# Kernel optimization log

Measured on AMD Instinct MI355X. Metric: run time of the kernel, lower is better.

## Reference

```python
import jax, jax.numpy as jnp
import numpy as np

B, S, D, H, L, V = 4, 1024, 1024, 16, 4, 32000
DH = D // H
DFF = 4 * D
PAD = 0
EPS = 1e-5


def setup_inputs() -> dict:
    key = jax.random.key(0)
    ks = jax.random.split(key, 10)
    std = 0.02
    inp = {
        'token_batch': jax.random.randint(ks[0], (B, S), 0, V),
        'E': jax.random.normal(ks[1], (V, D), jnp.float32) * std,
        'P': jax.random.normal(ks[2], (S, D), jnp.float32) * std,
        'Wq': jax.random.normal(ks[3], (L, H, D, DH), jnp.float32) * std,
        'bq': jnp.zeros((L, H, DH), jnp.float32),
        'Wk': jax.random.normal(ks[4], (L, H, D, DH), jnp.float32) * std,
        'bk': jnp.zeros((L, H, DH), jnp.float32),
        'Wv': jax.random.normal(ks[5], (L, H, D, DH), jnp.float32) * std,
        'bv': jnp.zeros((L, H, DH), jnp.float32),
        'W0': jax.random.normal(ks[6], (L, D, D), jnp.float32) * std,
        'b0': jnp.zeros((L, D), jnp.float32),
        'ln1_g': jnp.ones((L, D), jnp.float32),
        'ln1_b': jnp.zeros((L, D), jnp.float32),
        'ln2_g': jnp.ones((L, D), jnp.float32),
        'ln2_b': jnp.zeros((L, D), jnp.float32),
        'W1': jax.random.normal(ks[7], (L, D, DFF), jnp.float32) * std,
        'b1': jnp.zeros((L, DFF), jnp.float32),
        'W2': jax.random.normal(ks[8], (L, DFF, D), jnp.float32) * std,
        'b2': jnp.zeros((L, D), jnp.float32),
    }
    return inp


def _layernorm(x, g, b):
    m = jnp.mean(x, axis=-1, keepdims=True)
    v = jnp.mean(jnp.square(x - m), axis=-1, keepdims=True)
    return (x - m) * jax.lax.rsqrt(v + EPS) * g + b


def reference(token_batch, E, P, Wq, bq, Wk, bk, Wv, bv, W0, b0,
              ln1_g, ln1_b, ln2_g, ln2_b, W1, b1, W2, b2):
    scale = 1.0 / np.sqrt(DH)
    pad_mask = token_batch != PAD                         # [B,S]
    causal = jnp.tril(jnp.ones((S, S), bool))
    # combined causal + query-pad + key-pad mask, [B,S,S]
    mask = causal[None] & pad_mask[:, :, None] & pad_mask[:, None, :]

    X = E[token_batch] + P[None, :S]                      # [B,S,D] (dropout is eval no-op)

    def block(X, p):
        wq, bq_, wk, bk_, wv, bv_, w0, b0_, g1, be1, g2, be2, w1, bb1, w2, bb2 = p
        h = _layernorm(X, g1, be1)
        Q = jnp.einsum('bsd,hde->bhse', h, wq) + bq_[None, :, None, :]
        K = jnp.einsum('bsd,hde->bhse', h, wk) + bk_[None, :, None, :]
        Vv = jnp.einsum('bsd,hde->bhse', h, wv) + bv_[None, :, None, :]
        scores = jnp.einsum('bhse,bhte->bhst', Q, K) * scale
        scores = jnp.where(mask[:, None], scores, -1e9)
        w = jax.nn.softmax(scores, axis=-1)
        attn = jnp.einsum('bhst,bhte->bhse', w, Vv)       # [B,H,S,DH]
        attn = attn.transpose(0, 2, 1, 3).reshape(B, S, D)
        X = attn @ w0 + b0_ + X
        h = _layernorm(X, g2, be2)
        X = jax.nn.relu(h @ w1 + bb1) @ w2 + bb2 + X
        return X, None

    X, _ = jax.lax.scan(block, X, (Wq, bq, Wk, bk, Wv, bv, W0, b0,
                                   ln1_g, ln1_b, ln2_g, ln2_b, W1, b1, W2, b2))
    logits = X @ E.T                                      # tied-weight output head
    return logits
```

## Files before the change

### kernel.cpp

```cpp
#include <hip/hip_runtime.h>
#include <hip/hip_bf16.h>
#include <stdint.h>

#define BB   4
#define SS   1024
#define DD   1024
#define HH   16
#define LL   4
#define VV   32000
#define DHH  64
#define DFFN 4096
#define BSZ  4096

typedef __hip_bfloat16 bf16_t;
typedef _Float16 f16_t;
typedef __attribute__((ext_vector_type(8))) _Float16 f16x8;
typedef __attribute__((ext_vector_type(4))) float    f4v;

typedef __attribute__((address_space(1))) const void gvoid_t;
typedef __attribute__((address_space(3))) void       svoid_t;

static_assert(sizeof(f16_t) == 2, "f16 size");

__device__ __forceinline__ void gl2lds16(const f16_t* g, f16_t* l) {
  __builtin_amdgcn_global_load_lds(
      reinterpret_cast<gvoid_t*>(reinterpret_cast<uintptr_t>(g)),
      reinterpret_cast<svoid_t*>(static_cast<uint32_t>(reinterpret_cast<uintptr_t>(l))),
      16, 0, 0);
}

__device__ __forceinline__ float readf(const void* src, long i, int m) {
  if (m == 1) return __bfloat162float(((const bf16_t*)src)[i]);
  if (m == 2) return (float)((const f16_t*)src)[i];
  return ((const float*)src)[i];
}

__global__ void detect_k(const unsigned int* __restrict__ src, int* __restrict__ flag) {
  __shared__ int cnt;
  int tid = threadIdx.x;
  if (tid == 0) cnt = 0;
  __syncthreads();
  int c = 0;
  for (int i = tid; i < 1024; i += 256) {
    unsigned int w = src[i] & 0xffffu;
    unsigned int e = (w >> 7) & 0xffu;
    c += (e >= 96 && e <= 150) ? 1 : 0;
  }
  atomicAdd(&cnt, c);
  __syncthreads();
  if (tid == 0) *flag = (cnt >= 512) ? 1 : 0;
}

__global__ __launch_bounds__(256) void conv_f16_k(const void* __restrict__ src, f16_t* __restrict__ dst,
                                                  long n, const int* __restrict__ flag, int mode) {
  int m = (mode < 0) ? *flag : mode;
  long i = (long)blockIdx.x * blockDim.x + threadIdx.x;
  long stride = (long)gridDim.x * blockDim.x;
  for (; i < n; i += stride) dst[i] = (f16_t)readf(src, i, m);
}

__global__ __launch_bounds__(256) void conv_f32_k(const void* __restrict__ src, float* __restrict__ dst,
                                                  long n, const int* __restrict__ flag) {
  int m = *flag;
  long i = (long)blockIdx.x * blockDim.x + threadIdx.x;
  long stride = (long)gridDim.x * blockDim.x;
  for (; i < n; i += stride) dst[i] = readf(src, i, m);
}

__global__ __launch_bounds__(256) void transpose_k(const void* __restrict__ src, f16_t* __restrict__ dst,
                                                   int R, int C, const int* __restrict__ flag, int mode,
                                                   long dstL, int zper, long dstH) {
  int m = (mode < 0) ? *flag : mode;
  __shared__ float t[32][33];
  int tx = threadIdx.x, ty = threadIdx.y;
  long sbase = (long)blockIdx.z * R * C;
  long dbase = (long)(blockIdx.z / zper) * dstL + (long)(blockIdx.z % zper) * dstH;
  int c = blockIdx.x * 32 + tx;
#pragma unroll
  for (int i = 0; i < 4; ++i) {
    int r = blockIdx.y * 32 + ty + i * 8;
    t[ty + i * 8][tx] = (r < R && c < C) ? readf(src, sbase + (long)r * C + c, m) : 0.f;
  }
  __syncthreads();
#pragma unroll
  for (int i = 0; i < 4; ++i) {
    int oc = blockIdx.x * 32 + ty + i * 8;
    int orw = blockIdx.y * 32 + tx;
    if (oc < C && orw < R) dst[dbase + (long)oc * R + orw] = (f16_t)t[tx][ty + i * 8];
  }
}

__global__ __launch_bounds__(256) void embed_k(const int* __restrict__ tok, const f16_t* __restrict__ E,
                                               const f16_t* __restrict__ P, float* __restrict__ X) {
  int mrow = blockIdx.x;
  int s = mrow & (SS - 1);
  long eb = (long)tok[mrow] * DD;
  long pb = (long)s * DD;
  int d = threadIdx.x * 4;
  float4 o;
  o.x = (float)E[eb + d + 0] + (float)P[pb + d + 0];
  o.y = (float)E[eb + d + 1] + (float)P[pb + d + 1];
  o.z = (float)E[eb + d + 2] + (float)P[pb + d + 2];
  o.w = (float)E[eb + d + 3] + (float)P[pb + d + 3];
  ((float4*)(X + (long)mrow * DD))[threadIdx.x] = o;
}

__global__ __launch_bounds__(256) void ln_k(const float* __restrict__ X, const float* __restrict__ g,
                                            const float* __restrict__ be, f16_t* __restrict__ out) {
  __shared__ float red1[4], red2[4];
  int row = blockIdx.x, tid = threadIdx.x;
  float4 x = ((const float4*)(X + (long)row * DD))[tid];
  float s = x.x + x.y + x.z + x.w;
#pragma unroll
  for (int o = 32; o; o >>= 1) s += __shfl_down(s, o);
  if ((tid & 63) == 0) red1[tid >> 6] = s;
  __syncthreads();
  float mean = (red1[0] + red1[1] + red1[2] + red1[3]) * (1.f / DD);
  float d0 = x.x - mean, d1 = x.y - mean, d2 = x.z - mean, d3 = x.w - mean;
  float v = d0 * d0 + d1 * d1 + d2 * d2 + d3 * d3;
#pragma unroll
  for (int o = 32; o; o >>= 1) v += __shfl_down(v, o);
  if ((tid & 63) == 0) red2[tid >> 6] = v;
  __syncthreads();
  float rs = rsqrtf((red2[0] + red2[1] + red2[2] + red2[3]) * (1.f / DD) + 1e-5f);
  int d = tid * 4;
  union { ushort4 u4; f16_t h[4]; } o;
  o.h[0] = (f16_t)(d0 * rs * g[d + 0] + be[d + 0]);
  o.h[1] = (f16_t)(d1 * rs * g[d + 1] + be[d + 1]);
  o.h[2] = (f16_t)(d2 * rs * g[d + 2] + be[d + 2]);
  o.h[3] = (f16_t)(d3 * rs * g[d + 3] + be[d + 3]);
  ((ushort4*)(out + (long)row * DD))[tid] = o.u4;
}

__global__ __launch_bounds__(256) void softmax_k(const f16_t* __restrict__ sc, f16_t* __restrict__ pr,
                                                 const int* __restrict__ tok, int z0) {
  __shared__ float red1[4], red2[4];
  int s = blockIdx.x, zl = blockIdx.y, tid = threadIdx.x;
  int z = z0 + zl;
  int b = z & (BB - 1);
  const f16_t* srow = sc + ((long)zl * SS + s) * SS;
  f16_t* prow = pr + ((long)zl * SS + s) * SS;
  const int* tb = tok + b * SS;
  if (tb[s] == 0) {
    for (int k = tid; k < SS; k += 256) prow[k] = (f16_t)(1.0f / SS);
    return;
  }
  float val[4]; bool vld[4];
  float mx = -3e38f;
#pragma unroll
  for (int i = 0; i < 4; ++i) {
    int k = tid + i * 256;
    bool valid = (k <= s) && (tb[k] != 0);
    float v = valid ? (float)srow[k] * 0.125f : -3e38f;
    val[i] = v; vld[i] = valid;
    mx = fmaxf(mx, v);
  }
#pragma unroll
  for (int o = 32; o; o >>= 1) mx = fmaxf(mx, __shfl_down(mx, o));
  if ((tid & 63) == 0) red1[tid >> 6] = mx;
  __syncthreads();
  mx = fmaxf(fmaxf(red1[0], red1[1]), fmaxf(red1[2], red1[3]));
  float e[4]; float sum = 0.f;
#pragma unroll
  for (int i = 0; i < 4; ++i) { e[i] = vld[i] ? __expf(val[i] - mx) : 0.f; sum += e[i]; }
#pragma unroll
  for (int o = 32; o; o >>= 1) sum += __shfl_down(sum, o);
  if ((tid & 63) == 0) red2[tid >> 6] = sum;
  __syncthreads();
  float inv = 1.0f / (red2[0] + red2[1] + red2[2] + red2[3]);
#pragma unroll
  for (int i = 0; i < 4; ++i) prow[tid + i * 256] = (f16_t)(e[i] * inv);
}

struct GemmP {
  const f16_t* A; const f16_t* B; void* C;
  int M, N, K, lda, ldb, ldc;
  long sAz, sBz;
  int z0, zdiv, czmode;
  long sCz1, sCz2;
  const float* bias;
  long bstr;
  const float* resid;
  const int* flag;
};

template <int EPI, bool SKIPU, int BN>
__global__ __launch_bounds__(256) void gemm_bt(GemmP p) {
  int bx = blockIdx.x, by = blockIdx.y, bz = blockIdx.z;
  if (SKIPU && bx > by) return;
  constexpr int NJ = BN / 32;
  __shared__ __align__(16) f16_t la[128 * 32];
  __shared__ __align__(16) f16_t lb[BN * 32];
  int tid = threadIdx.x;
  const f16_t* Ab = p.A + (long)bz * p.sAz;
  const f16_t* Bb = p.B + (long)bz * p.sBz;

  int r0 = tid >> 2;
  int c8 = (tid & 3) << 3;
  long ar0 = (long)by * 128 + r0;
  long ar1 = ar0 + 64;
  int brow0 = bx * BN + r0;      if (brow0 > p.N - 1) brow0 = p.N - 1;
  const f16_t* ag0 = Ab + ar0 * p.lda + c8;
  const f16_t* ag1 = Ab + ar1 * p.lda + c8;
  const f16_t* bg0 = Bb + (long)brow0 * p.ldb + c8;
  const f16_t* bg1 = nullptr;
  if constexpr (BN == 128) {
    int brow1 = bx * BN + 64 + r0; if (brow1 > p.N - 1) brow1 = p.N - 1;
    bg1 = Bb + (long)brow1 * p.ldb + c8;
  }
  f16_t* la0 = la + tid * 8; f16_t* la1 = la + 2048 + tid * 8;
  f16_t* lb0 = lb + tid * 8; f16_t* lb1 = lb + 2048 + tid * 8;

  int w = tid >> 6, l = tid & 63;
  int wm = (w >> 1) << 6, wn = (w & 1) * (BN / 2);
  int lr = l & 15, q = l >> 4;

  f4v acc[4][NJ];
  f4v zero = {0.f, 0.f, 0.f, 0.f};
#pragma unroll
  for (int i = 0; i < 4; ++i)
#pragma unroll
    for (int j = 0; j < NJ; ++j) acc[i][j] = zero;

  int nk = p.K >> 5;
  for (int kt = 0; kt < nk; ++kt) {
    __syncthreads();
    long ko = (long)kt << 5;
    gl2lds16(ag0 + ko, la0);
    gl2lds16(ag1 + ko, la1);
    gl2lds16(bg0 + ko, lb0);
    if constexpr (BN == 128) gl2lds16(bg1 + ko, lb1);
    __syncthreads();
    f16x8 af[4], bfr[NJ];
#pragma unroll
    for (int i = 0; i < 4; ++i) af[i] = *(const f16x8*)(la + (wm + i * 16 + lr) * 32 + q * 8);
#pragma unroll
    for (int j = 0; j < NJ; ++j) bfr[j] = *(const f16x8*)(lb + (wn + j * 16 + lr) * 32 + q * 8);
#pragma unroll
    for (int i = 0; i < 4; ++i)
#pragma unroll
      for (int j = 0; j < NJ; ++j)
        acc[i][j] = __builtin_amdgcn_mfma_f32_16x16x32_f16(af[i], bfr[j], acc[i][j], 0, 0, 0);
  }

  long cz;
  if (p.czmode == 1) { int z = p.z0 + bz; cz = (long)(z / p.zdiv) * p.sCz1 + (long)(z % p.zdiv) * p.sCz2; }
  else cz = (long)bz * p.sCz2;
  int flg = 0;
  if constexpr (EPI == 6) flg = *p.flag;

#pragma unroll
  for (int i = 0; i < 4; ++i) {
    int gr0 = by * 128 + wm + i * 16 + q * 4;
#pragma unroll
    for (int j = 0; j < NJ; ++j) {
      int gc = bx * BN + wn + j * 16 + lr;
      if (gc >= p.N) continue;
      float bv = 0.f;
      if constexpr (EPI == 1) bv = p.bias[(long)(gc >> 10) * p.bstr + (gc & (DD - 1))];
      if constexpr (EPI == 3 || EPI == 4) bv = p.bias[gc];
#pragma unroll
      for (int r = 0; r < 4; ++r) {
        int row = gr0 + r;
        if (row >= p.M) continue;
        float v = acc[i][j][r];
        if constexpr (EPI == 0) {
          ((float*)p.C)[cz + (long)row * p.ldc + gc] = v;
        } else if constexpr (EPI == 1) {
          long ad = ((long)(gc >> 6) * p.M + row) * 64 + (gc & 63);
          ((f16_t*)p.C)[ad] = (f16_t)(v + bv);
        } else if constexpr (EPI == 2) {
          ((f16_t*)p.C)[cz + (long)row * p.ldc + gc] = (f16_t)v;
        } else if constexpr (EPI == 3) {
          long ad = cz + (long)row * p.ldc + gc;
          ((float*)p.C)[ad] = v + bv + p.resid[ad];
        } else if constexpr (EPI == 4) {
          float t = v + bv; t = t > 0.f ? t : 0.f;
          ((f16_t*)p.C)[cz + (long)row * p.ldc + gc] = (f16_t)t;
        } else if constexpr (EPI == 6) {
          long ad = cz + (long)row * p.ldc + gc;
          if (flg) ((bf16_t*)p.C)[ad] = __float2bfloat16(v);
          else     ((float*)p.C)[ad] = v;
        }
      }
    }
  }
}

extern "C" void kernel_launch(void* const* d_in, const int* in_sizes, int n_in,
                              void* d_out, int out_size, void* d_ws, size_t ws_size,
                              hipStream_t stream) {
  (void)in_sizes; (void)n_in; (void)out_size;
  const int*  tok = (const int*)d_in[0];
  const void* E_  = d_in[1];  const void* P_  = d_in[2];
  const void* Wq_ = d_in[3];  const void* bq_ = d_in[4];
  const void* Wk_ = d_in[5];  const void* bk_ = d_in[6];
  const void* Wv_ = d_in[7];  const void* bv_ = d_in[8];
  const void* W0_ = d_in[9];  const void* b0_ = d_in[10];
  const void* g1_ = d_in[11]; const void* be1_ = d_in[12];
  const void* g2_ = d_in[13]; const void* be2_ = d_in[14];
  const void* W1_ = d_in[15]; const void* b1_ = d_in[16];
  const void* W2_ = d_in[17]; const void* b2_ = d_in[18];

  char* wsb = (char*)d_ws;
  size_t off = 0;
  auto alloc = [&](size_t bytes) -> void* {
    off = (off + 255) & ~(size_t)255;
    void* p = wsb + off;
    off += bytes;
    return p;
  };

  int*    flag  = (int*)alloc(4);
  f16_t*  Ef    = (f16_t*)alloc((size_t)VV * DD * 2);
  f16_t*  Pf    = (f16_t*)alloc((size_t)SS * DD * 2);
  f16_t*  Wqkvt = (f16_t*)alloc((size_t)LL * 3 * DD * DD * 2);
  f16_t*  W0t   = (f16_t*)alloc((size_t)LL * DD * DD * 2);
  f16_t*  W1t   = (f16_t*)alloc((size_t)LL * DFFN * DD * 2);
  f16_t*  W2t   = (f16_t*)alloc((size_t)LL * DD * DFFN * 2);
  float*  bqkvf = (float*)alloc((size_t)3 * LL * HH * DHH * 4);
  float*  b0f   = (float*)alloc((size_t)LL * DD * 4);
  float*  b1f   = (float*)alloc((size_t)LL * DFFN * 4);
  float*  b2f   = (float*)alloc((size_t)LL * DD * 4);
  float*  g1f   = (float*)alloc((size_t)LL * DD * 4);
  float*  be1f  = (float*)alloc((size_t)LL * DD * 4);
  float*  g2f   = (float*)alloc((size_t)LL * DD * 4);
  float*  be2f  = (float*)alloc((size_t)LL * DD * 4);
  float*  X     = (float*)alloc((size_t)BSZ * DD * 4);
  f16_t*  hbuf  = (f16_t*)alloc((size_t)BSZ * DD * 2);
  f16_t*  QKVb  = (f16_t*)alloc((size_t)3 * HH * BB * SS * DHH * 2);
  f16_t*  Vt    = (f16_t*)alloc((size_t)HH * BB * DHH * SS * 2);
  f16_t*  attn  = (f16_t*)alloc((size_t)BSZ * DD * 2);
  f16_t*  ff    = (f16_t*)alloc((size_t)BSZ * DFFN * 2);

  f16_t* Qb = QKVb;
  f16_t* Kb = QKVb + (size_t)HH * BB * SS * DHH;
  f16_t* Vb = QKVb + (size_t)2 * HH * BB * SS * DHH;

  size_t rem = ws_size > off ? ws_size - off : 0;
  int CH = 64;
  while (CH > 1 && ((size_t)CH * SS * SS * 2 + 1024) > rem) CH >>= 1;
  f16_t* scoresB = (f16_t*)alloc((size_t)CH * SS * SS * 2);

  dim3 blk(256);

  detect_k<<<dim3(1), blk, 0, stream>>>((const unsigned int*)E_, flag);
  conv_f16_k<<<dim3(8192), blk, 0, stream>>>(E_, Ef, (long)VV * DD, flag, -1);
  conv_f16_k<<<dim3(1024), blk, 0, stream>>>(P_, Pf, (long)SS * DD, flag, -1);
  conv_f32_k<<<dim3(16), blk, 0, stream>>>(bq_, bqkvf, (long)LL * HH * DHH, flag);
  conv_f32_k<<<dim3(16), blk, 0, stream>>>(bk_, bqkvf + (size_t)LL * HH * DHH, (long)LL * HH * DHH, flag);
  conv_f32_k<<<dim3(16), blk, 0, stream>>>(bv_, bqkvf + (size_t)2 * LL * HH * DHH, (long)LL * HH * DHH, flag);
  conv_f32_k<<<dim3(16), blk, 0, stream>>>(b0_, b0f, (long)LL * DD, flag);
  conv_f32_k<<<dim3(64), blk, 0, stream>>>(b1_, b1f, (long)LL * DFFN, flag);
  conv_f32_k<<<dim3(16), blk, 0, stream>>>(b2_, b2f, (long)LL * DD, flag);
  conv_f32_k<<<dim3(16), blk, 0, stream>>>(g1_, g1f, (long)LL * DD, flag);
  conv_f32_k<<<dim3(16), blk, 0, stream>>>(be1_, be1f, (long)LL * DD, flag);
  conv_f32_k<<<dim3(16), blk, 0, stream>>>(g2_, g2f, (long)LL * DD, flag);
  conv_f32_k<<<dim3(16), blk, 0, stream>>>(be2_, be2f, (long)LL * DD, flag);

  const long W3 = (long)3 * DD * DD;
  transpose_k<<<dim3(2, 32, LL * HH), dim3(32, 8), 0, stream>>>(Wq_, Wqkvt + 0 * DD * DD, DD, DHH, flag, -1,
                                                                W3, HH, (long)DHH * DD);
  transpose_k<<<dim3(2, 32, LL * HH), dim3(32, 8), 0, stream>>>(Wk_, Wqkvt + 1 * DD * DD, DD, DHH, flag, -1,
                                                                W3, HH, (long)DHH * DD);
  transpose_k<<<dim3(2, 32, LL * HH), dim3(32, 8), 0, stream>>>(Wv_, Wqkvt + 2 * DD * DD, DD, DHH, flag, -1,
                                                                W3, HH, (long)DHH * DD);
  transpose_k<<<dim3(32, 32, LL), dim3(32, 8), 0, stream>>>(W0_, W0t, DD, DD, flag, -1,
                                                            (long)DD * DD, 1, 0);
  transpose_k<<<dim3(128, 32, LL), dim3(32, 8), 0, stream>>>(W1_, W1t, DD, DFFN, flag, -1,
                                                             (long)DD * DFFN, 1, 0);
  transpose_k<<<dim3(32, 128, LL), dim3(32, 8), 0, stream>>>(W2_, W2t, DFFN, DD, flag, -1,
                                                             (long)DFFN * DD, 1, 0);

  embed_k<<<dim3(BSZ), blk, 0, stream>>>(tok, Ef, Pf, X);

  for (int l = 0; l < LL; ++l) {
    ln_k<<<dim3(BSZ), blk, 0, stream>>>(X, g1f + (long)l * DD, be1f + (long)l * DD, hbuf);

    GemmP pq{};
    pq.A = hbuf; pq.lda = DD; pq.M = BSZ; pq.N = 3 * DD; pq.K = DD;
    pq.B = Wqkvt + (long)l * W3; pq.ldb = DD; pq.ldc = 0;
    pq.sAz = 0; pq.sBz = 0;
    pq.z0 = 0; pq.zdiv = 1; pq.czmode = 0; pq.sCz1 = 0; pq.sCz2 = 0;
    pq.C = QKVb; pq.bias = bqkvf + (long)l * HH * DHH; pq.bstr = (long)LL * HH * DHH;
    pq.resid = nullptr; pq.flag = nullptr;
    gemm_bt<1, false, 128><<<dim3(24, 32, 1), blk, 0, stream>>>(pq);

    transpose_k<<<dim3(2, 32, HH * BB), dim3(32, 8), 0, stream>>>((const void*)Vb, Vt, SS, DHH, nullptr, 2,
                                                                  (long)DHH * SS, 1, 0);

    int nch = (HH * BB) / CH;
    for (int c = 0; c < nch; ++c) {
      int z0 = c * CH;
      GemmP ps{};
      ps.A = Qb + (long)z0 * SS * DHH; ps.sAz = (long)SS * DHH; ps.lda = DHH;
      ps.B = Kb + (long)z0 * SS * DHH; ps.sBz = (long)SS * DHH; ps.ldb = DHH;
      ps.M = SS; ps.N = SS; ps.K = DHH;
      ps.C = scoresB; ps.ldc = SS; ps.czmode = 0; ps.z0 = 0; ps.zdiv = 1;
      ps.sCz1 = 0; ps.sCz2 = (long)SS * SS;
      ps.bias = nullptr; ps.bstr = 0; ps.resid = nullptr; ps.flag = nullptr;
      gemm_bt<2, true, 128><<<dim3(8, 8, CH), blk, 0, stream>>>(ps);

      softmax_k<<<dim3(SS, CH), blk, 0, stream>>>(scoresB, scoresB, tok, z0);

      GemmP pp{};
      pp.A = scoresB; pp.sAz = (long)SS * SS; pp.lda = SS;
      pp.B = Vt + (long)z0 * DHH * SS; pp.sBz = (long)DHH * SS; pp.ldb = SS;
      pp.M = SS; pp.N = DHH; pp.K = SS;
      pp.C = attn; pp.ldc = DD; pp.czmode = 1; pp.z0 = z0; pp.zdiv = BB;
      pp.sCz1 = DHH; pp.sCz2 = (long)SS * DD;
      pp.bias = nullptr; pp.bstr = 0; pp.resid = nullptr; pp.flag = nullptr;
      gemm_bt<2, false, 64><<<dim3(1, 8, CH), blk, 0, stream>>>(pp);
    }

    GemmP p0{};
    p0.A = attn; p0.lda = DD; p0.M = BSZ; p0.N = DD; p0.K = DD;
    p0.B = W0t + (long)l * DD * DD; p0.ldb = DD;
    p0.C = X; p0.ldc = DD; p0.czmode = 0; p0.z0 = 0; p0.zdiv = 1;
    p0.sAz = 0; p0.sBz = 0; p0.sCz1 = 0; p0.sCz2 = 0;
    p0.bias = b0f + (long)l * DD; p0.bstr = 0; p0.resid = X; p0.flag = nullptr;
    gemm_bt<3, false, 128><<<dim3(8, 32, 1), blk, 0, stream>>>(p0);

    ln_k<<<dim3(BSZ), blk, 0, stream>>>(X, g2f + (long)l * DD, be2f + (long)l * DD, hbuf);

    GemmP p1{};
    p1.A = hbuf; p1.lda = DD; p1.M = BSZ; p1.N = DFFN; p1.K = DD;
    p1.B = W1t + (long)l * DFFN * DD; p1.ldb = DD;
    p1.C = ff; p1.ldc = DFFN; p1.czmode = 0; p1.z0 = 0; p1.zdiv = 1;
    p1.sAz = 0; p1.sBz = 0; p1.sCz1 = 0; p1.sCz2 = 0;
    p1.bias = b1f + (long)l * DFFN; p1.bstr = 0; p1.resid = nullptr; p1.flag = nullptr;
    gemm_bt<4, false, 128><<<dim3(32, 32, 1), blk, 0, stream>>>(p1);

    GemmP p2{};
    p2.A = ff; p2.lda = DFFN; p2.M = BSZ; p2.N = DD; p2.K = DFFN;
    p2.B = W2t + (long)l * DD * DFFN; p2.ldb = DFFN;
    p2.C = X; p2.ldc = DD; p2.czmode = 0; p2.z0 = 0; p2.zdiv = 1;
    p2.sAz = 0; p2.sBz = 0; p2.sCz1 = 0; p2.sCz2 = 0;
    p2.bias = b2f + (long)l * DD; p2.bstr = 0; p2.resid = X; p2.flag = nullptr;
    gemm_bt<3, false, 128><<<dim3(8, 32, 1), blk, 0, stream>>>(p2);
  }

  conv_f16_k<<<dim3(4096), blk, 0, stream>>>((const void*)X, hbuf, (long)BSZ * DD, flag, 0);
  GemmP pl{};
  pl.A = hbuf; pl.lda = DD; pl.M = BSZ; pl.N = VV; pl.K = DD;
  pl.B = Ef; pl.ldb = DD;
  pl.C = d_out; pl.ldc = VV; pl.czmode = 0; pl.z0 = 0; pl.zdiv = 1;
  pl.sAz = 0; pl.sBz = 0; pl.sCz1 = 0; pl.sCz2 = 0;
  pl.bias = nullptr; pl.bstr = 0; pl.resid = nullptr; pl.flag = flag;
  gemm_bt<6, false, 128><<<dim3(250, 32, 1), blk, 0, stream>>>(pl);
}
```

Baseline: 3.163 ms.

## Add 256x256 eight-wave pipelined GEMM for QKV, FFN1 and logits

Adds a new 512-thread GEMM kernel with 256x256 output tiles, XOR-swizzled LDS, a double-buffered ping-pong schedule that interleaves global-to-LDS loads with MFMA quarters, and s_setprio around the math. It is used for the QKV projection, the FFN up-projection and the large vocabulary logits GEMM. It also adds XCD-aware workgroup remapping to both the old and new GEMMs for better L2 locality. The aim is higher tensor-core utilisation and less load latency exposure, at the cost of 128KB dynamic LDS and a hand-tuned barrier schedule that assumes M, N and K divide the tile sizes.

```diff
diff --git a/kernel.cpp b/kernel.cpp
--- a/kernel.cpp
+++ b/kernel.cpp
@@ -187,6 +187,14 @@
 template <int EPI, bool SKIPU, int BN>
 __global__ __launch_bounds__(256) void gemm_bt(GemmP p) {
   int bx = blockIdx.x, by = blockIdx.y, bz = blockIdx.z;
+  if (gridDim.z == 1) {
+    int n = gridDim.x * gridDim.y;
+    if ((n & 7) == 0) {
+      int wg = bx + gridDim.x * by;
+      int s = (wg & 7) * (n >> 3) + (wg >> 3);
+      by = s % gridDim.y; bx = s / gridDim.y;
+    }
+  }
   if (SKIPU && bx > by) return;
   constexpr int NJ = BN / 32;
   __shared__ __align__(16) f16_t la[128 * 32];
@@ -246,8 +254,6 @@
   long cz;
   if (p.czmode == 1) { int z = p.z0 + bz; cz = (long)(z / p.zdiv) * p.sCz1 + (long)(z % p.zdiv) * p.sCz2; }
   else cz = (long)bz * p.sCz2;
-  int flg = 0;
-  if constexpr (EPI == 6) flg = *p.flag;
 
 #pragma unroll
   for (int i = 0; i < 4; ++i) {
@@ -257,7 +263,6 @@
       int gc = bx * BN + wn + j * 16 + lr;
       if (gc >= p.N) continue;
       float bv = 0.f;
-      if constexpr (EPI == 1) bv = p.bias[(long)(gc >> 10) * p.bstr + (gc & (DD - 1))];
       if constexpr (EPI == 3 || EPI == 4) bv = p.bias[gc];
 #pragma unroll
       for (int r = 0; r < 4; ++r) {
@@ -266,9 +271,6 @@
         float v = acc[i][j][r];
         if constexpr (EPI == 0) {
           ((float*)p.C)[cz + (long)row * p.ldc + gc] = v;
-        } else if constexpr (EPI == 1) {
-          long ad = ((long)(gc >> 6) * p.M + row) * 64 + (gc & 63);
-          ((f16_t*)p.C)[ad] = (f16_t)(v + bv);
         } else if constexpr (EPI == 2) {
           ((f16_t*)p.C)[cz + (long)row * p.ldc + gc] = (f16_t)v;
         } else if constexpr (EPI == 3) {
@@ -277,8 +279,176 @@
         } else if constexpr (EPI == 4) {
           float t = v + bv; t = t > 0.f ? t : 0.f;
           ((f16_t*)p.C)[cz + (long)row * p.ldc + gc] = (f16_t)t;
+        }
+      }
+    }
+  }
+}
+
+struct Gemm8P {
+  const f16_t* A; const f16_t* B; void* C;
+  int M, N, K, lda, ldb, ldc;
+  const float* bias;
+  long bstr;
+  const int* flag;
+};
+
+#define BARR()  asm volatile("s_barrier" ::: "memory")
+#define WAITL0() do { asm volatile("s_waitcnt lgkmcnt(0)" ::: "memory"); __builtin_amdgcn_sched_barrier(0); } while (0)
+#define WVM(n)  asm volatile("s_waitcnt vmcnt(" n ")" ::: "memory")
+
+template <int EPI>
+__global__ __launch_bounds__(512, 2) void gemm8p(Gemm8P p) {
+  extern __shared__ __align__(16) f16_t lds[];
+  constexpr int A0 = 0, A1 = 16384, B0 = 32768, B1 = 49152;
+  int tid = threadIdx.x;
+
+  int nwg = gridDim.x * gridDim.y;
+  int wg = blockIdx.x + gridDim.x * blockIdx.y;
+  int s = (wg & 7) * (nwg >> 3) + (wg >> 3);
+  int by = s % gridDim.y;
+  int bx = s / gridDim.y;
+
+  int wave = tid >> 6, l = tid & 63;
+  int wr = wave >> 2, wc = wave & 3;
+  int lr = l & 15, q = l >> 4;
+
+  int r8 = tid >> 3, ch = tid & 7;
+  int chs = ch ^ (r8 & 7);
+  const f16_t* pA = p.A + ((long)by * 256 + r8) * p.lda + chs * 8;
+  const f16_t* pB = p.B + ((long)bx * 256 + r8) * p.ldb + chs * 8;
+  f16_t* ldsw = lds + tid * 8;
+
+  auto SA = [&](int t, int h, int off) {
+    const f16_t* g = pA + ((long)h * 128) * p.lda + (long)t * 64;
+    gl2lds16(g, ldsw + off);
+    gl2lds16(g + (long)64 * p.lda, ldsw + off + 4096);
+  };
+  auto SB = [&](int t, int h, int off) {
+    const f16_t* g = pB + ((long)h * 128) * p.ldb + (long)t * 64;
+    gl2lds16(g, ldsw + off);
+    gl2lds16(g + (long)64 * p.ldb, ldsw + off + 4096);
+  };
+
+  f16x8 afr[4][2], bfr[2][2][2];
+  auto LA = [&](int off, int qm) {
+#pragma unroll
+    for (int i = 0; i < 4; ++i) {
+      int row = wr * 128 + qm * 64 + i * 16 + lr;
+#pragma unroll
+      for (int ks = 0; ks < 2; ++ks) {
+        int c = ks * 4 + q;
+        afr[i][ks] = *(const f16x8*)(lds + off + row * 64 + ((c ^ (lr & 7)) << 3));
+      }
+    }
+  };
+  auto LB = [&](int off, int qn) {
+#pragma unroll
+    for (int j = 0; j < 2; ++j) {
+      int row = wc * 64 + qn * 32 + j * 16 + lr;
+#pragma unroll
+      for (int ks = 0; ks < 2; ++ks) {
+        int c = ks * 4 + q;
+        bfr[qn][j][ks] = *(const f16x8*)(lds + off + row * 64 + ((c ^ (lr & 7)) << 3));
+      }
+    }
+  };
+
+  f4v acc[8][4];
+  f4v zero = {0.f, 0.f, 0.f, 0.f};
+#pragma unroll
+  for (int i = 0; i < 8; ++i)
+#pragma unroll
+    for (int j = 0; j < 4; ++j) acc[i][j] = zero;
+
+  auto MM = [&](int qm, int qn) {
+#pragma unroll
+    for (int i = 0; i < 4; ++i)
+#pragma unroll
+      for (int j = 0; j < 2; ++j)
+#pragma unroll
+        for (int ks = 0; ks < 2; ++ks)
+          acc[qm * 4 + i][qn * 2 + j] =
+              __builtin_amdgcn_mfma_f32_16x16x32_f16(afr[i][ks], bfr[qn][j][ks],
+                                                     acc[qm * 4 + i][qn * 2 + j], 0, 0, 0);
+  };
+
+  int npair = p.K >> 7;
+
+  SB(0, 0, B0); SB(0, 1, B0 + 8192);
+  SA(0, 0, A0); SA(0, 1, A0 + 8192);
+  SB(1, 0, B1); SB(1, 1, B1 + 8192);
+  WVM("4"); BARR();
+
+  for (int kp = 0; kp < npair; ++kp) {
+    int t1 = 2 * kp + 1, t2 = 2 * kp + 2, t3 = 2 * kp + 3;
+    bool nl = (kp != npair - 1);
+    LA(A0, 0); LB(B0, 0);
+    SA(t1, 0, A1);
+    BARR(); WAITL0();
+    __builtin_amdgcn_s_setprio(1); MM(0, 0); __builtin_amdgcn_s_setprio(0);
+    BARR();
+    LB(B0, 1);
+    SA(t1, 1, A1 + 8192);
+    BARR(); WAITL0();
+    __builtin_amdgcn_s_setprio(1); MM(0, 1); __builtin_amdgcn_s_setprio(0);
+    BARR();
+    LA(A0, 1);
+    if (nl) SB(t2, 0, B0);
+    BARR(); WAITL0();
+    __builtin_amdgcn_s_setprio(1); MM(1, 1); __builtin_amdgcn_s_setprio(0);
+    BARR();
+    if (nl) SB(t2, 1, B0 + 8192);
+    BARR();
+    __builtin_amdgcn_s_setprio(1); MM(1, 0); __builtin_amdgcn_s_setprio(0);
+    if (nl) { WVM("4"); } else { WVM("0"); }
+    BARR();
+    LA(A1, 0); LB(B1, 0);
+    if (nl) SA(t2, 0, A0);
+    BARR(); WAITL0();
+    __builtin_amdgcn_s_setprio(1); MM(0, 0); __builtin_amdgcn_s_setprio(0);
+    BARR();
+    LB(B1, 1);
+    if (nl) SA(t2, 1, A0 + 8192);
+    BARR(); WAITL0();
+    __builtin_amdgcn_s_setprio(1); MM(0, 1); __builtin_amdgcn_s_setprio(0);
+    BARR();
+    LA(A1, 1);
+    if (nl) SB(t3, 0, B1);
+    BARR(); WAITL0();
+    __builtin_amdgcn_s_setprio(1); MM(1, 1); __builtin_amdgcn_s_setprio(0);
+    BARR();
+    if (nl) SB(t3, 1, B1 + 8192);
+    BARR();
+    __builtin_amdgcn_s_setprio(1); MM(1, 0); __builtin_amdgcn_s_setprio(0);
+    if (nl) WVM("4");
+    BARR();
+  }
+
+  int flg = 0;
+  if constexpr (EPI == 6) flg = *p.flag;
+
+#pragma unroll
+  for (int mi = 0; mi < 8; ++mi) {
+    int grow = by * 256 + wr * 128 + mi * 16 + q * 4;
+#pragma unroll
+    for (int ni = 0; ni < 4; ++ni) {
+      int gc = bx * 256 + wc * 64 + ni * 16 + lr;
+      float bv = 0.f;
+      if constexpr (EPI == 1) bv = p.bias[(long)(gc >> 10) * p.bstr + (gc & (DD - 1))];
+      if constexpr (EPI == 4) bv = p.bias[gc];
+#pragma unroll
+      for (int r = 0; r < 4; ++r) {
+        int row = grow + r;
+        float v = acc[mi][ni][r];
+        if constexpr (EPI == 1) {
+          long ad = ((long)(gc >> 6) * p.M + row) * 64 + (gc & 63);
+          ((f16_t*)p.C)[ad] = (f16_t)(v + bv);
+        } else if constexpr (EPI == 4) {
+          float t = v + bv; t = t > 0.f ? t : 0.f;
+          ((f16_t*)p.C)[(long)row * p.ldc + gc] = (f16_t)t;
         } else if constexpr (EPI == 6) {
-          long ad = cz + (long)row * p.ldc + gc;
+          long ad = (long)row * p.ldc + gc;
           if (flg) ((bf16_t*)p.C)[ad] = __float2bfloat16(v);
           else     ((float*)p.C)[ad] = v;
         }
@@ -301,6 +471,13 @@
   const void* g2_ = d_in[13]; const void* be2_ = d_in[14];
   const void* W1_ = d_in[15]; const void* b1_ = d_in[16];
   const void* W2_ = d_in[17]; const void* b2_ = d_in[18];
+
+  (void)hipFuncSetAttribute(reinterpret_cast<const void*>(&gemm8p<1>),
+                            hipFuncAttributeMaxDynamicSharedMemorySize, 131072);
+  (void)hipFuncSetAttribute(reinterpret_cast<const void*>(&gemm8p<4>),
+                            hipFuncAttributeMaxDynamicSharedMemorySize, 131072);
+  (void)hipFuncSetAttribute(reinterpret_cast<const void*>(&gemm8p<6>),
+                            hipFuncAttributeMaxDynamicSharedMemorySize, 131072);
 
   char* wsb = (char*)d_ws;
   size_t off = 0;
@@ -377,14 +554,11 @@
   for (int l = 0; l < LL; ++l) {
     ln_k<<<dim3(BSZ), blk, 0, stream>>>(X, g1f + (long)l * DD, be1f + (long)l * DD, hbuf);
 
-    GemmP pq{};
-    pq.A = hbuf; pq.lda = DD; pq.M = BSZ; pq.N = 3 * DD; pq.K = DD;
-    pq.B = Wqkvt + (long)l * W3; pq.ldb = DD; pq.ldc = 0;
-    pq.sAz = 0; pq.sBz = 0;
-    pq.z0 = 0; pq.zdiv = 1; pq.czmode = 0; pq.sCz1 = 0; pq.sCz2 = 0;
-    pq.C = QKVb; pq.bias = bqkvf + (long)l * HH * DHH; pq.bstr = (long)LL * HH * DHH;
-    pq.resid = nullptr; pq.flag = nullptr;
-    gemm_bt<1, false, 128><<<dim3(24, 32, 1), blk, 0, stream>>>(pq);
+    Gemm8P q8{};
+    q8.A = hbuf; q8.B = Wqkvt + (long)l * W3; q8.C = QKVb;
+    q8.M = BSZ; q8.N = 3 * DD; q8.K = DD; q8.lda = DD; q8.ldb = DD; q8.ldc = 0;
+    q8.bias = bqkvf + (long)l * HH * DHH; q8.bstr = (long)LL * HH * DHH; q8.flag = nullptr;
+    gemm8p<1><<<dim3(12, 16), dim3(512), 131072, stream>>>(q8);
 
     transpose_k<<<dim3(2, 32, HH * BB), dim3(32, 8), 0, stream>>>((const void*)Vb, Vt, SS, DHH, nullptr, 2,
                                                                   (long)DHH * SS, 1, 0);
@@ -423,13 +597,11 @@
 
     ln_k<<<dim3(BSZ), blk, 0, stream>>>(X, g2f + (long)l * DD, be2f + (long)l * DD, hbuf);
 
-    GemmP p1{};
-    p1.A = hbuf; p1.lda = DD; p1.M = BSZ; p1.N = DFFN; p1.K = DD;
-    p1.B = W1t + (long)l * DFFN * DD; p1.ldb = DD;
-    p1.C = ff; p1.ldc = DFFN; p1.czmode = 0; p1.z0 = 0; p1.zdiv = 1;
-    p1.sAz = 0; p1.sBz = 0; p1.sCz1 = 0; p1.sCz2 = 0;
-    p1.bias = b1f + (long)l * DFFN; p1.bstr = 0; p1.resid = nullptr; p1.flag = nullptr;
-    gemm_bt<4, false, 128><<<dim3(32, 32, 1), blk, 0, stream>>>(p1);
+    Gemm8P f8{};
+    f8.A = hbuf; f8.B = W1t + (long)l * DFFN * DD; f8.C = ff;
+    f8.M = BSZ; f8.N = DFFN; f8.K = DD; f8.lda = DD; f8.ldb = DD; f8.ldc = DFFN;
+    f8.bias = b1f + (long)l * DFFN; f8.bstr = 0; f8.flag = nullptr;
+    gemm8p<4><<<dim3(16, 16), dim3(512), 131072, stream>>>(f8);
 
     GemmP p2{};
     p2.A = ff; p2.lda = DFFN; p2.M = BSZ; p2.N = DD; p2.K = DFFN;
@@ -441,11 +613,9 @@
   }
 
   conv_f16_k<<<dim3(4096), blk, 0, stream>>>((const void*)X, hbuf, (long)BSZ * DD, flag, 0);
-  GemmP pl{};
-  pl.A = hbuf; pl.lda = DD; pl.M = BSZ; pl.N = VV; pl.K = DD;
-  pl.B = Ef; pl.ldb = DD;
-  pl.C = d_out; pl.ldc = VV; pl.czmode = 0; pl.z0 = 0; pl.zdiv = 1;
-  pl.sAz = 0; pl.sBz = 0; pl.sCz1 = 0; pl.sCz2 = 0;
-  pl.bias = nullptr; pl.bstr = 0; pl.resid = nullptr; pl.flag = flag;
-  gemm_bt<6, false, 128><<<dim3(250, 32, 1), blk, 0, stream>>>(pl);
-}
+  Gemm8P pl{};
+  pl.A = hbuf; pl.B = Ef; pl.C = d_out;
+  pl.M = BSZ; pl.N = VV; pl.K = DD; pl.lda = DD; pl.ldb = DD; pl.ldc = VV;
+  pl.bias = nullptr; pl.bstr = 0; pl.flag = flag;
+  gemm8p<6><<<dim3(125, 16), dim3(512), 131072, stream>>>(pl);
+}
```

Result: faster. 2.820 ms (-10.8%).
